# Kernel optimization log

Hardware: AMD Instinct MI355X
Metric: run time of the kernel (lower is better)

Reference implementation:

```python
import jax, jax.numpy as jnp
import numpy as np

TOP_K = 2
ROUTE_SCALE = 1.0
EPS = 1e-20

B, S, D = 2, 512, 1024
E = 8            # num_experts
F = 768          # moe_intermediate_size
FS = 768 * 1     # shared expert intermediate (moe_intermediate_size * num_shared_experts)


def setup_inputs() -> dict:
    key = jax.random.key(0)
    ks = jax.random.split(key, 9)
    s = 0.02
    return {
        "hidden_states": jax.random.normal(ks[0], (B, S, D), dtype=jnp.float32),
        "W_gate_router": jax.random.normal(ks[1], (D, E), dtype=jnp.float32) * s,
        "expert_bias": jnp.zeros((E,), dtype=jnp.float32),
        "Wg": jax.random.normal(ks[2], (E, D, F), dtype=jnp.float32) * s,
        "Wu": jax.random.normal(ks[3], (E, D, F), dtype=jnp.float32) * s,
        "Wd": jax.random.normal(ks[4], (E, F, D), dtype=jnp.float32) * s,
        "Wg_s": jax.random.normal(ks[5], (D, FS), dtype=jnp.float32) * s,
        "Wu_s": jax.random.normal(ks[6], (D, FS), dtype=jnp.float32) * s,
        "Wd_s": jax.random.normal(ks[7], (FS, D), dtype=jnp.float32) * s,
    }


def reference(hidden_states, W_gate_router, expert_bias, Wg, Wu, Wd, Wg_s, Wu_s, Wd_s):
    b, s, d = hidden_states.shape
    x = hidden_states.reshape(-1, d)                      # [T, D]
    T = x.shape[0]

    # ---- token-choice top-k router (sigmoid scoring, route_norm) ----
    logits = x @ W_gate_router                            # [T, E]
    scores = jax.nn.sigmoid(logits.astype(jnp.float32))   # [T, E] fp32
    _, sel = jax.lax.top_k(scores + expert_bias, TOP_K)   # [T, K] (bias only for selection)
    top_scores = jnp.take_along_axis(scores, sel, axis=1)  # [T, K]
    top_scores = top_scores / (top_scores.sum(-1, keepdims=True) + EPS)  # route_norm
    top_scores = top_scores * ROUTE_SCALE

    # ---- shared expert (always active) ----
    shared = (jax.nn.silu(x @ Wg_s) * (x @ Wu_s)) @ Wd_s  # [T, D]

    # ---- dispatch: N = T*K routed slots (scatter-add is order-independent,
    #      so the torch stable-argsort grouping is mathematically a no-op) ----
    tok = jnp.repeat(jnp.arange(T), TOP_K)                # [N] source token per slot
    exp = sel.reshape(-1)                                 # [N] expert per slot
    w = top_scores.reshape(-1)                            # [N]
    xr = x[tok]                                           # [N, D]

    # per-expert SiLU-GLU MLP, vectorized over experts then select own expert's row
    h = jax.nn.silu(jnp.einsum('nd,edf->enf', xr, Wg)) * jnp.einsum('nd,edf->enf', xr, Wu)
    out_all = jnp.einsum('enf,efd->end', h, Wd)           # [E, N, D]
    routed = out_all[exp, jnp.arange(exp.shape[0])]       # [N, D]
    routed = (routed.astype(jnp.float32) * w[:, None]).astype(hidden_states.dtype)

    # ---- combine: scatter-add routed outputs onto shared output ----
    out = shared.at[tok].add(routed)                      # [T, D]
    return out.reshape(b, s, d)
```

## Files before the change

kernel.cpp:

```cpp
#include <hip/hip_runtime.h>
#include <hip/hip_bf16.h>
#include <math.h>

#define T_TOK   1024
#define D_DIM   1024
#define E_NUM   8
#define F_DIM   768
#define N_SLOTS 2048

typedef unsigned short u16;
typedef unsigned int   u32;
typedef __attribute__((ext_vector_type(8))) short bf16x8;
typedef __attribute__((ext_vector_type(4))) float f32x4;

#define WS_SEL    0
#define WS_WTS    8192
#define WS_BUCKET 16384
#define WS_COUNTS 49152
#define WS_OFFS   49216
#define WS_POS    49280
#define WS_XB     65536
#define WS_H      (WS_XB + 2097152)
#define WS_Y      (WS_H + 4718592)

__device__ __forceinline__ u16 f2bf(float x) {
    u32 u = __float_as_uint(x);
    u += 0x7fffu + ((u >> 16) & 1u);
    return (u16)(u >> 16);
}
#define PKBF(hi, lo) __builtin_amdgcn_perm(__float_as_uint(hi), __float_as_uint(lo), 0x07060302u)

__device__ __forceinline__ int physB(int r, int c) {
    return r * 64 + ((c ^ (r & 7)) << 3);
}

__global__ __launch_bounds__(256) void xrouter_kernel(
    const float* __restrict__ X, const float* __restrict__ Wr,
    const float* __restrict__ bias, u16* __restrict__ Xb,
    int* __restrict__ sel, float* __restrict__ wts)
{
    int t = blockIdx.x * 4 + (threadIdx.x >> 6);
    int lane = threadIdx.x & 63;
    const float* xrow = X + (size_t)t * D_DIM;
    u16* brow = Xb + (size_t)t * D_DIM;
    float acc[E_NUM];
#pragma unroll
    for (int e = 0; e < E_NUM; ++e) acc[e] = 0.f;
#pragma unroll
    for (int q = 0; q < 4; ++q) {
        int d = q * 256 + lane * 4;
        float4 v = *(const float4*)(xrow + d);
        ushort4 o;
        o.x = f2bf(v.x); o.y = f2bf(v.y); o.z = f2bf(v.z); o.w = f2bf(v.w);
        *(ushort4*)(brow + d) = o;
        const float xv[4] = {v.x, v.y, v.z, v.w};
#pragma unroll
        for (int jj = 0; jj < 4; ++jj) {
            const float4* wr = (const float4*)(Wr + (size_t)(d + jj) * E_NUM);
            float4 w0 = wr[0], w1 = wr[1];
            acc[0] += xv[jj] * w0.x; acc[1] += xv[jj] * w0.y;
            acc[2] += xv[jj] * w0.z; acc[3] += xv[jj] * w0.w;
            acc[4] += xv[jj] * w1.x; acc[5] += xv[jj] * w1.y;
            acc[6] += xv[jj] * w1.z; acc[7] += xv[jj] * w1.w;
        }
    }
#pragma unroll
    for (int e = 0; e < E_NUM; ++e)
#pragma unroll
        for (int off = 32; off > 0; off >>= 1)
            acc[e] += __shfl_xor(acc[e], off);
    if (lane == 0) {
        float s[E_NUM], b[E_NUM];
#pragma unroll
        for (int e = 0; e < E_NUM; ++e) {
            s[e] = 1.f / (1.f + expf(-acc[e]));
            b[e] = s[e] + bias[e];
        }
        int i1 = 0; float b1 = b[0];
#pragma unroll
        for (int e = 1; e < E_NUM; ++e) if (b[e] > b1) { b1 = b[e]; i1 = e; }
        int i2 = -1; float b2 = -INFINITY;
#pragma unroll
        for (int e = 0; e < E_NUM; ++e) {
            if (e == i1) continue;
            if (b[e] > b2) { b2 = b[e]; i2 = e; }
        }
        float s1 = s[i1], s2 = s[i2];
        float denom = s1 + s2 + 1e-20f;
        sel[2 * t] = i1; sel[2 * t + 1] = i2;
        wts[2 * t] = s1 / denom; wts[2 * t + 1] = s2 / denom;
    }
}

__global__ __launch_bounds__(512) void dispatch_kernel(
    const int* __restrict__ sel, int* __restrict__ bucket,
    int* __restrict__ counts, int* __restrict__ offs, int* __restrict__ pos)
{
    __shared__ int soffs[E_NUM + 1];
    int e = threadIdx.x >> 6;
    int lane = threadIdx.x & 63;
    int running = 0;
    for (int base = 0; base < N_SLOTS; base += 64) {
        int slot = base + lane;
        bool mine = (sel[slot] == e);
        unsigned long long mask = __ballot(mine);
        if (mine) {
            int rank = running + __popcll(mask & ((1ull << lane) - 1ull));
            bucket[e * T_TOK + rank] = slot;
        }
        running += __popcll(mask);
    }
    if (lane == 0) counts[e] = running;
    __syncthreads();
    if (threadIdx.x == 0) {
        int o = 0;
        for (int k = 0; k < E_NUM; ++k) { soffs[k] = o; offs[k] = o; o += counts[k]; }
        soffs[E_NUM] = o; offs[E_NUM] = o;
    }
    __syncthreads();
    int base_off = soffs[e];
    for (int r = lane; r < running; r += 64)
        pos[bucket[e * T_TOK + r]] = base_off + r;
}

__global__ __launch_bounds__(256, 4) void proj1(
    const u16* __restrict__ Xb,
    const float* __restrict__ Wg, const float* __restrict__ Wu,
    const float* __restrict__ Wgs, const float* __restrict__ Wus,
    u16* __restrict__ H,
    const int* __restrict__ bucket, const int* __restrict__ counts, const int* __restrict__ offs)
{
    const int i = blockIdx.x;
    const int cxcd = i & 7, m = i >> 3;
    const int y = m & 31, phi = m >> 5;
    const int panel = phi * 8 + cxcd;
    if (panel >= 108) return;
    const int unit = panel / 12, x = panel - unit * 12;

    int nrows, rbase; const float *Bg, *Bu;
    if (unit < E_NUM) {
        nrows = counts[unit]; rbase = offs[unit];
        Bg = Wg + (size_t)unit * D_DIM * F_DIM;
        Bu = Wu + (size_t)unit * D_DIM * F_DIM;
    } else { nrows = T_TOK; rbase = N_SLOTS; Bg = Wgs; Bu = Wus; }
    const int row0 = y * 32;
    if (row0 >= nrows) return;

    __shared__ u16 smem[2][160 * 64];

    const int t = threadIdx.x;
    const int wv = t >> 6, lane = t & 63, l15 = lane & 15, g = lane >> 4;

    const int ar = t >> 3, ac = t & 7;
    int grow = min(row0 + ar, nrows - 1);
    if (unit < E_NUM) grow = bucket[unit * T_TOK + grow] >> 1;
    const u16* srcA = Xb + (size_t)grow * D_DIM + ac * 8;
    const int wA = physB(ar, ac);

    const int bn = t & 127, bh = t >> 7;
    const float* srcB = ((bn < 64) ? Bg : Bu) + (size_t)(bh * 32) * F_DIM + x * 64 + (bn & 63);
    int wB[4];
#pragma unroll
    for (int q = 0; q < 4; ++q)
        wB[q] = physB(32 + bn, bh * 4 + q);

    f32x4 accg[2], accu[2];
    const f32x4 z4 = {0.f, 0.f, 0.f, 0.f};
#pragma unroll
    for (int ri = 0; ri < 2; ++ri) { accg[ri] = z4; accu[ri] = z4; }

    uint4 pa;
    float pb[32];
#define LOAD1(kt) do { \
    pa = *(const uint4*)(srcA + (kt)); \
    const float* _bp = srcB + (size_t)(kt) * F_DIM; \
    _Pragma("unroll") \
    for (int ii = 0; ii < 32; ++ii) pb[ii] = _bp[(size_t)ii * F_DIM]; \
} while (0)
#define WRITE1(buf) do { \
    *(uint4*)&smem[buf][wA] = pa; \
    _Pragma("unroll") \
    for (int q = 0; q < 4; ++q) { \
        u32 pk[4]; \
        _Pragma("unroll") \
        for (int j = 0; j < 4; ++j) pk[j] = PKBF(pb[8*q + 2*j + 1], pb[8*q + 2*j]); \
        *(uint4*)&smem[buf][wB[q]] = *(const uint4*)pk; \
    } \
} while (0)
#define COMP1(buf) do { \
    const u16* _p = smem[buf]; \
    _Pragma("unroll") \
    for (int kk = 0; kk < 2; ++kk) { \
        bf16x8 _a[2], _bg, _bu; \
        _Pragma("unroll") \
        for (int ri = 0; ri < 2; ++ri) { \
            int rr = ri * 16 + l15; \
            _a[ri] = *(const bf16x8*)&_p[rr * 64 + ((((kk << 2) | g) ^ (rr & 7)) << 3)]; \
        } \
        { \
            int rg = 32 + wv * 16 + l15; \
            _bg = *(const bf16x8*)&_p[rg * 64 + ((((kk << 2) | g) ^ (rg & 7)) << 3)]; \
            int ru = rg + 64; \
            _bu = *(const bf16x8*)&_p[ru * 64 + ((((kk << 2) | g) ^ (ru & 7)) << 3)]; \
        } \
        _Pragma("unroll") \
        for (int ri = 0; ri < 2; ++ri) { \
            accg[ri] = __builtin_amdgcn_mfma_f32_16x16x32_bf16(_a[ri], _bg, accg[ri], 0, 0, 0); \
            accu[ri] = __builtin_amdgcn_mfma_f32_16x16x32_bf16(_a[ri], _bu, accu[ri], 0, 0, 0); \
        } \
    } \
} while (0)

    LOAD1(0);
    for (int tt = 0; tt < 16; ++tt) {
        WRITE1(tt & 1);
        if (tt + 1 < 16) LOAD1((tt + 1) * 64);
        __syncthreads();
        COMP1(tt & 1);
    }
#undef LOAD1
#undef WRITE1
#undef COMP1

#pragma unroll
    for (int ri = 0; ri < 2; ++ri) {
        int n = x * 64 + wv * 16 + l15;
#pragma unroll
        for (int r = 0; r < 4; ++r) {
            int row = row0 + ri * 16 + g * 4 + r;
            if (row >= nrows) continue;
            float gv = accg[ri][r];
            float uv = accu[ri][r];
            H[(size_t)(rbase + row) * F_DIM + n] =
                f2bf(gv / (1.f + __expf(-gv)) * uv);
        }
    }
}

__global__ __launch_bounds__(256, 3) void proj2(
    const u16* __restrict__ H,
    const float* __restrict__ Wd, const float* __restrict__ Wds,
    float* __restrict__ Y,
    const int* __restrict__ counts, const int* __restrict__ offs)
{
    const int i = blockIdx.x;
    const int cxcd = i & 7, m = i >> 3;
    const int y = m & 31, phi = m >> 5;
    const int panel = phi * 8 + cxcd;
    const int unit = panel >> 4, x = panel & 15;

    int nrows, rbase; const float* Bm;
    if (unit < E_NUM) {
        nrows = counts[unit]; rbase = offs[unit];
        Bm = Wd + (size_t)unit * F_DIM * D_DIM;
    } else { nrows = T_TOK; rbase = N_SLOTS; Bm = Wds; }
    const int row0 = y * 64;
    if (row0 >= nrows) return;

    __shared__ u16 smem[2][128 * 64];

    const int t = threadIdx.x;
    const int wv = t >> 6, lane = t & 63, l15 = lane & 15, g = lane >> 4;
    const int wm = wv >> 1, wn = wv & 1;

    const int ar = t >> 2, ac = t & 3;
    const int grow = rbase + min(row0 + ar, nrows - 1);
    const u16* srcA = H + (size_t)grow * F_DIM + ac * 8;
    const int wA0 = ar * 64 + ((ac     ^ (ar & 7)) * 8);
    const int wA1 = ar * 64 + (((ac+4) ^ (ar & 7)) * 8);

    const int bn = t & 63;
    const int bq = t >> 6;
    const float* srcB = Bm + (size_t)(bq * 16) * D_DIM + x * 64 + bn;
    int wB[2];
#pragma unroll
    for (int q = 0; q < 2; ++q)
        wB[q] = (64 + bn) * 64 + (((bq * 2 + q) ^ (bn & 7)) * 8);

    f32x4 acc[2][2];
    const f32x4 z4 = {0.f, 0.f, 0.f, 0.f};
#pragma unroll
    for (int ri = 0; ri < 2; ++ri)
#pragma unroll
        for (int ci = 0; ci < 2; ++ci) acc[ri][ci] = z4;

    uint4 pa0, pa1;
    float pb[16];
#define LOAD2(kt) do { \
    pa0 = *(const uint4*)(srcA + (kt)); \
    pa1 = *(const uint4*)(srcA + (kt) + 32); \
    const float* _bp = srcB + (size_t)(kt) * D_DIM; \
    _Pragma("unroll") \
    for (int ii = 0; ii < 16; ++ii) pb[ii] = _bp[(size_t)ii * D_DIM]; \
} while (0)
#define WRITE2(buf) do { \
    *(uint4*)&smem[buf][wA0] = pa0; \
    *(uint4*)&smem[buf][wA1] = pa1; \
    _Pragma("unroll") \
    for (int q = 0; q < 2; ++q) { \
        u32 pk[4]; \
        _Pragma("unroll") \
        for (int j = 0; j < 4; ++j) pk[j] = PKBF(pb[8*q + 2*j + 1], pb[8*q + 2*j]); \
        *(uint4*)&smem[buf][wB[q]] = *(const uint4*)pk; \
    } \
} while (0)
#define COMP2(buf) do { \
    const u16* _p = smem[buf]; \
    _Pragma("unroll") \
    for (int kk = 0; kk < 2; ++kk) { \
        const int ch = (((kk << 2) | g) ^ (l15 & 7)) * 8; \
        bf16x8 _a[2], _b[2]; \
        _Pragma("unroll") \
        for (int ri = 0; ri < 2; ++ri) \
            _a[ri] = *(const bf16x8*)&_p[(wm * 32 + ri * 16 + l15) * 64 + ch]; \
        _Pragma("unroll") \
        for (int ci = 0; ci < 2; ++ci) \
            _b[ci] = *(const bf16x8*)&_p[(64 + wn * 32 + ci * 16 + l15) * 64 + ch]; \
        _Pragma("unroll") \
        for (int ri = 0; ri < 2; ++ri) \
            _Pragma("unroll") \
            for (int ci = 0; ci < 2; ++ci) \
                acc[ri][ci] = __builtin_amdgcn_mfma_f32_16x16x32_bf16(_a[ri], _b[ci], acc[ri][ci], 0, 0, 0); \
    } \
} while (0)

    LOAD2(0);
    for (int tt = 0; tt < 12; ++tt) {
        WRITE2(tt & 1);
        if (tt + 1 < 12) LOAD2((tt + 1) * 64);
        __syncthreads();
        COMP2(tt & 1);
    }
#undef LOAD2
#undef WRITE2
#undef COMP2

#pragma unroll
    for (int ri = 0; ri < 2; ++ri)
#pragma unroll
        for (int ci = 0; ci < 2; ++ci) {
            int n = x * 64 + wn * 32 + ci * 16 + l15;
#pragma unroll
            for (int r = 0; r < 4; ++r) {
                int row = row0 + wm * 32 + ri * 16 + g * 4 + r;
                if (row >= nrows) continue;
                Y[(size_t)(rbase + row) * D_DIM + n] = acc[ri][ci][r];
            }
        }
}

__global__ __launch_bounds__(256) void combine_kernel(
    const float* __restrict__ Y, const int* __restrict__ pos,
    const float* __restrict__ wts, float* __restrict__ out)
{
    int t = blockIdx.x;
    int d = threadIdx.x * 4;
    int p0 = pos[2 * t], p1 = pos[2 * t + 1];
    float w0 = wts[2 * t], w1 = wts[2 * t + 1];
    float4 a = *(const float4*)(Y + (size_t)(N_SLOTS + t) * D_DIM + d);
    float4 b = *(const float4*)(Y + (size_t)p0 * D_DIM + d);
    float4 cc = *(const float4*)(Y + (size_t)p1 * D_DIM + d);
    float4 o;
    o.x = a.x + w0 * b.x + w1 * cc.x;
    o.y = a.y + w0 * b.y + w1 * cc.y;
    o.z = a.z + w0 * b.z + w1 * cc.z;
    o.w = a.w + w0 * b.w + w1 * cc.w;
    *(float4*)(out + (size_t)t * D_DIM + d) = o;
}

extern "C" void kernel_launch(void* const* d_in, const int* in_sizes, int n_in,
                              void* d_out, int out_size, void* d_ws, size_t ws_size,
                              hipStream_t stream) {
    const float* X    = (const float*)d_in[0];
    const float* Wr   = (const float*)d_in[1];
    const float* bias = (const float*)d_in[2];
    const float* Wg   = (const float*)d_in[3];
    const float* Wu   = (const float*)d_in[4];
    const float* Wd   = (const float*)d_in[5];
    const float* Wgs  = (const float*)d_in[6];
    const float* Wus  = (const float*)d_in[7];
    const float* Wds  = (const float*)d_in[8];
    float* out = (float*)d_out;

    char* ws = (char*)d_ws;
    int*   sel    = (int*)(ws + WS_SEL);
    float* wtsv   = (float*)(ws + WS_WTS);
    int*   bucket = (int*)(ws + WS_BUCKET);
    int*   counts = (int*)(ws + WS_COUNTS);
    int*   offs   = (int*)(ws + WS_OFFS);
    int*   pos    = (int*)(ws + WS_POS);
    u16*   Xb     = (u16*)(ws + WS_XB);
    u16*   H      = (u16*)(ws + WS_H);
    float* Y      = (float*)(ws + WS_Y);

    xrouter_kernel<<<256, 256, 0, stream>>>(X, Wr, bias, Xb, sel, wtsv);
    dispatch_kernel<<<1, 512, 0, stream>>>(sel, bucket, counts, offs, pos);

    proj1<<<3584, 256, 0, stream>>>(Xb, Wg, Wu, Wgs, Wus, H, bucket, counts, offs);
    proj2<<<4608, 256, 0, stream>>>(H, Wd, Wds, Y, counts, offs);
    combine_kernel<<<T_TOK, 256, 0, stream>>>(Y, pos, wtsv, out);
}
```

Baseline: 92.25 us.

## Swap GEMM operand roles with weight-stationary tiles and async LDS token loads

Both expert GEMMs are restructured so each block owns a weight column slice and a 256-token tile, with the weights as the small M operand and tokens as N. Token activations are copied straight into LDS with global_load_lds, and the fp32 weight loads overlap compute in a reordered double-buffer loop. Per-block tiles grow a lot (fewer blocks, more accumulators, vectorized stores), cutting how often the fp32 weights are re-read across token tiles. The cost is lower occupancy, larger LDS use, and idle waves in partially filled expert tiles.

```diff
diff --git a/kernel.cpp b/kernel.cpp
--- a/kernel.cpp
+++ b/kernel.cpp
@@ -32,6 +32,12 @@
 
 __device__ __forceinline__ int physB(int r, int c) {
     return r * 64 + ((c ^ (r & 7)) << 3);
+}
+
+__device__ __forceinline__ void async16(const void* gp, void* sp) {
+    __builtin_amdgcn_global_load_lds(
+        (const __attribute__((address_space(1))) unsigned int*)gp,
+        (__attribute__((address_space(3))) unsigned int*)sp, 16, 0, 0);
 }
 
 __global__ __launch_bounds__(256) void xrouter_kernel(
@@ -123,19 +129,19 @@
         pos[bucket[e * T_TOK + r]] = base_off + r;
 }
 
-__global__ __launch_bounds__(256, 4) void proj1(
+__global__ __launch_bounds__(256, 2) void proj1(
     const u16* __restrict__ Xb,
     const float* __restrict__ Wg, const float* __restrict__ Wu,
     const float* __restrict__ Wgs, const float* __restrict__ Wus,
     u16* __restrict__ H,
-    const int* __restrict__ bucket, const int* __restrict__ counts, const int* __restrict__ offs)
+    const int* __restrict__ bucket, const int* __restrict__ counts,
+    const int* __restrict__ offs)
 {
     const int i = blockIdx.x;
-    const int cxcd = i & 7, m = i >> 3;
-    const int y = m & 31, phi = m >> 5;
-    const int panel = phi * 8 + cxcd;
-    if (panel >= 108) return;
-    const int unit = panel / 12, x = panel - unit * 12;
+    const int unit = i / 96;
+    const int rem = i - unit * 96;
+    const int x = rem >> 2;
+    const int nt = rem & 3;
 
     int nrows, rbase; const float *Bg, *Bu;
     if (unit < E_NUM) {
@@ -143,209 +149,217 @@
         Bg = Wg + (size_t)unit * D_DIM * F_DIM;
         Bu = Wu + (size_t)unit * D_DIM * F_DIM;
     } else { nrows = T_TOK; rbase = N_SLOTS; Bg = Wgs; Bu = Wus; }
-    const int row0 = y * 32;
-    if (row0 >= nrows) return;
-
-    __shared__ u16 smem[2][160 * 64];
-
-    const int t = threadIdx.x;
-    const int wv = t >> 6, lane = t & 63, l15 = lane & 15, g = lane >> 4;
-
-    const int ar = t >> 3, ac = t & 7;
-    int grow = min(row0 + ar, nrows - 1);
-    if (unit < E_NUM) grow = bucket[unit * T_TOK + grow] >> 1;
-    const u16* srcA = Xb + (size_t)grow * D_DIM + ac * 8;
-    const int wA = physB(ar, ac);
-
-    const int bn = t & 127, bh = t >> 7;
-    const float* srcB = ((bn < 64) ? Bg : Bu) + (size_t)(bh * 32) * F_DIM + x * 64 + (bn & 63);
-    int wB[4];
-#pragma unroll
-    for (int q = 0; q < 4; ++q)
-        wB[q] = physB(32 + bn, bh * 4 + q);
-
-    f32x4 accg[2], accu[2];
+    const int tbase = nt * 256;
+    if (tbase >= nrows) return;
+
+    __shared__ u16 smem[2][320 * 64];
+
+    const int t = threadIdx.x, wv = t >> 6, lane = t & 63, l15 = lane & 15, g = lane >> 4;
+
+    const float* srcA = ((lane < 32) ? Bg : Bu) + (size_t)(wv * 16) * F_DIM + x * 32 + (lane & 31);
+    const int wA0 = physB(lane, 2 * wv);
+    const int wA1 = physB(lane, 2 * wv + 1);
+
+    const u16* srcB[8];
+#pragma unroll
+    for (int j = 0; j < 8; ++j) {
+        int tl = wv * 64 + j * 8 + (lane >> 3);
+        int tok = min(tbase + tl, nrows - 1);
+        int grow = (unit < E_NUM) ? (bucket[unit * T_TOK + tok] >> 1) : tok;
+        srcB[j] = Xb + (size_t)grow * D_DIM + (((lane & 7) ^ (lane >> 3)) << 3);
+    }
+
+    f32x4 accg[2][4], accu[2][4];
     const f32x4 z4 = {0.f, 0.f, 0.f, 0.f};
 #pragma unroll
-    for (int ri = 0; ri < 2; ++ri) { accg[ri] = z4; accu[ri] = z4; }
-
-    uint4 pa;
-    float pb[32];
-#define LOAD1(kt) do { \
-    pa = *(const uint4*)(srcA + (kt)); \
-    const float* _bp = srcB + (size_t)(kt) * F_DIM; \
-    _Pragma("unroll") \
-    for (int ii = 0; ii < 32; ++ii) pb[ii] = _bp[(size_t)ii * F_DIM]; \
-} while (0)
-#define WRITE1(buf) do { \
-    *(uint4*)&smem[buf][wA] = pa; \
-    _Pragma("unroll") \
-    for (int q = 0; q < 4; ++q) { \
-        u32 pk[4]; \
-        _Pragma("unroll") \
-        for (int j = 0; j < 4; ++j) pk[j] = PKBF(pb[8*q + 2*j + 1], pb[8*q + 2*j]); \
-        *(uint4*)&smem[buf][wB[q]] = *(const uint4*)pk; \
-    } \
+    for (int mi = 0; mi < 2; ++mi)
+#pragma unroll
+        for (int ni = 0; ni < 4; ++ni) { accg[mi][ni] = z4; accu[mi][ni] = z4; }
+
+    float pa[16];
+#define ASYNCB1(kt, buf) do { \
+    _Pragma("unroll") \
+    for (int j = 0; j < 8; ++j) \
+        async16(srcB[j] + (kt), &smem[buf][(64 + wv * 64 + j * 8) * 64]); \
+} while (0)
+#define LOADA1(kt) do { \
+    const float* _s = srcA + (size_t)(kt) * F_DIM; \
+    _Pragma("unroll") \
+    for (int j = 0; j < 16; ++j) pa[j] = _s[(size_t)j * F_DIM]; \
+} while (0)
+#define WRITEA1(buf) do { \
+    u32 pk[8]; \
+    _Pragma("unroll") \
+    for (int j = 0; j < 8; ++j) pk[j] = PKBF(pa[2*j + 1], pa[2*j]); \
+    *(uint4*)&smem[buf][wA0] = *(const uint4*)&pk[0]; \
+    *(uint4*)&smem[buf][wA1] = *(const uint4*)&pk[4]; \
 } while (0)
 #define COMP1(buf) do { \
     const u16* _p = smem[buf]; \
     _Pragma("unroll") \
     for (int kk = 0; kk < 2; ++kk) { \
-        bf16x8 _a[2], _bg, _bu; \
-        _Pragma("unroll") \
-        for (int ri = 0; ri < 2; ++ri) { \
-            int rr = ri * 16 + l15; \
-            _a[ri] = *(const bf16x8*)&_p[rr * 64 + ((((kk << 2) | g) ^ (rr & 7)) << 3)]; \
+        const int ch = (((kk << 2) | g) ^ (l15 & 7)) << 3; \
+        bf16x8 _ag[2], _au[2], _b[4]; \
+        _Pragma("unroll") \
+        for (int mi = 0; mi < 2; ++mi) { \
+            _ag[mi] = *(const bf16x8*)&_p[(mi * 16 + l15) * 64 + ch]; \
+            _au[mi] = *(const bf16x8*)&_p[(32 + mi * 16 + l15) * 64 + ch]; \
         } \
-        { \
-            int rg = 32 + wv * 16 + l15; \
-            _bg = *(const bf16x8*)&_p[rg * 64 + ((((kk << 2) | g) ^ (rg & 7)) << 3)]; \
-            int ru = rg + 64; \
-            _bu = *(const bf16x8*)&_p[ru * 64 + ((((kk << 2) | g) ^ (ru & 7)) << 3)]; \
-        } \
-        _Pragma("unroll") \
-        for (int ri = 0; ri < 2; ++ri) { \
-            accg[ri] = __builtin_amdgcn_mfma_f32_16x16x32_bf16(_a[ri], _bg, accg[ri], 0, 0, 0); \
-            accu[ri] = __builtin_amdgcn_mfma_f32_16x16x32_bf16(_a[ri], _bu, accu[ri], 0, 0, 0); \
-        } \
+        _Pragma("unroll") \
+        for (int ni = 0; ni < 4; ++ni) \
+            _b[ni] = *(const bf16x8*)&_p[(64 + wv * 64 + ni * 16 + l15) * 64 + ch]; \
+        _Pragma("unroll") \
+        for (int mi = 0; mi < 2; ++mi) \
+            _Pragma("unroll") \
+            for (int ni = 0; ni < 4; ++ni) { \
+                accg[mi][ni] = __builtin_amdgcn_mfma_f32_16x16x32_bf16(_ag[mi], _b[ni], accg[mi][ni], 0, 0, 0); \
+                accu[mi][ni] = __builtin_amdgcn_mfma_f32_16x16x32_bf16(_au[mi], _b[ni], accu[mi][ni], 0, 0, 0); \
+            } \
     } \
 } while (0)
 
-    LOAD1(0);
+    ASYNCB1(0, 0);
+    LOADA1(0);
+    WRITEA1(0);
+    __syncthreads();
     for (int tt = 0; tt < 16; ++tt) {
-        WRITE1(tt & 1);
-        if (tt + 1 < 16) LOAD1((tt + 1) * 64);
+        const int cb = tt & 1, nb = cb ^ 1;
+        if (tt + 1 < 16) { ASYNCB1((tt + 1) * 64, nb); LOADA1((tt + 1) * 64); }
+        COMP1(cb);
+        if (tt + 1 < 16) WRITEA1(nb);
         __syncthreads();
-        COMP1(tt & 1);
-    }
-#undef LOAD1
-#undef WRITE1
+    }
+#undef ASYNCB1
+#undef LOADA1
+#undef WRITEA1
 #undef COMP1
 
 #pragma unroll
-    for (int ri = 0; ri < 2; ++ri) {
-        int n = x * 64 + wv * 16 + l15;
-#pragma unroll
-        for (int r = 0; r < 4; ++r) {
-            int row = row0 + ri * 16 + g * 4 + r;
-            if (row >= nrows) continue;
-            float gv = accg[ri][r];
-            float uv = accu[ri][r];
-            H[(size_t)(rbase + row) * F_DIM + n] =
-                f2bf(gv / (1.f + __expf(-gv)) * uv);
-        }
-    }
-}
-
-__global__ __launch_bounds__(256, 3) void proj2(
+    for (int mi = 0; mi < 2; ++mi)
+#pragma unroll
+        for (int ni = 0; ni < 4; ++ni) {
+            int token = tbase + wv * 64 + ni * 16 + l15;
+            if (token >= nrows) continue;
+            int f0 = x * 32 + mi * 16 + g * 4;
+            ushort4 hv;
+            float gv, uv;
+            gv = accg[mi][ni][0]; uv = accu[mi][ni][0];
+            hv.x = f2bf(gv / (1.f + __expf(-gv)) * uv);
+            gv = accg[mi][ni][1]; uv = accu[mi][ni][1];
+            hv.y = f2bf(gv / (1.f + __expf(-gv)) * uv);
+            gv = accg[mi][ni][2]; uv = accu[mi][ni][2];
+            hv.z = f2bf(gv / (1.f + __expf(-gv)) * uv);
+            gv = accg[mi][ni][3]; uv = accu[mi][ni][3];
+            hv.w = f2bf(gv / (1.f + __expf(-gv)) * uv);
+            *(ushort4*)(H + (size_t)(rbase + token) * F_DIM + f0) = hv;
+        }
+}
+
+__global__ __launch_bounds__(256, 2) void proj2(
     const u16* __restrict__ H,
     const float* __restrict__ Wd, const float* __restrict__ Wds,
     float* __restrict__ Y,
     const int* __restrict__ counts, const int* __restrict__ offs)
 {
     const int i = blockIdx.x;
-    const int cxcd = i & 7, m = i >> 3;
-    const int y = m & 31, phi = m >> 5;
-    const int panel = phi * 8 + cxcd;
-    const int unit = panel >> 4, x = panel & 15;
+    const int unit = i / 64;
+    const int rem = i - unit * 64;
+    const int x = rem >> 2;
+    const int nt = rem & 3;
 
     int nrows, rbase; const float* Bm;
     if (unit < E_NUM) {
         nrows = counts[unit]; rbase = offs[unit];
         Bm = Wd + (size_t)unit * F_DIM * D_DIM;
     } else { nrows = T_TOK; rbase = N_SLOTS; Bm = Wds; }
-    const int row0 = y * 64;
-    if (row0 >= nrows) return;
-
-    __shared__ u16 smem[2][128 * 64];
-
-    const int t = threadIdx.x;
-    const int wv = t >> 6, lane = t & 63, l15 = lane & 15, g = lane >> 4;
-    const int wm = wv >> 1, wn = wv & 1;
-
-    const int ar = t >> 2, ac = t & 3;
-    const int grow = rbase + min(row0 + ar, nrows - 1);
-    const u16* srcA = H + (size_t)grow * F_DIM + ac * 8;
-    const int wA0 = ar * 64 + ((ac     ^ (ar & 7)) * 8);
-    const int wA1 = ar * 64 + (((ac+4) ^ (ar & 7)) * 8);
-
-    const int bn = t & 63;
-    const int bq = t >> 6;
-    const float* srcB = Bm + (size_t)(bq * 16) * D_DIM + x * 64 + bn;
-    int wB[2];
-#pragma unroll
-    for (int q = 0; q < 2; ++q)
-        wB[q] = (64 + bn) * 64 + (((bq * 2 + q) ^ (bn & 7)) * 8);
-
-    f32x4 acc[2][2];
+    const int tbase = nt * 256;
+    if (tbase >= nrows) return;
+
+    __shared__ u16 smem[2][320 * 64];
+
+    const int t = threadIdx.x, wv = t >> 6, lane = t & 63, l15 = lane & 15, g = lane >> 4;
+
+    const float* srcA = Bm + (size_t)(wv * 16) * D_DIM + x * 64 + lane;
+    const int wA0 = physB(lane, 2 * wv);
+    const int wA1 = physB(lane, 2 * wv + 1);
+
+    const u16* srcB[8];
+#pragma unroll
+    for (int j = 0; j < 8; ++j) {
+        int tl = wv * 64 + j * 8 + (lane >> 3);
+        int tok = min(tbase + tl, nrows - 1);
+        srcB[j] = H + (size_t)(rbase + tok) * F_DIM + (((lane & 7) ^ (lane >> 3)) << 3);
+    }
+
+    f32x4 acc[4][4];
     const f32x4 z4 = {0.f, 0.f, 0.f, 0.f};
 #pragma unroll
-    for (int ri = 0; ri < 2; ++ri)
-#pragma unroll
-        for (int ci = 0; ci < 2; ++ci) acc[ri][ci] = z4;
-
-    uint4 pa0, pa1;
-    float pb[16];
-#define LOAD2(kt) do { \
-    pa0 = *(const uint4*)(srcA + (kt)); \
-    pa1 = *(const uint4*)(srcA + (kt) + 32); \
-    const float* _bp = srcB + (size_t)(kt) * D_DIM; \
-    _Pragma("unroll") \
-    for (int ii = 0; ii < 16; ++ii) pb[ii] = _bp[(size_t)ii * D_DIM]; \
-} while (0)
-#define WRITE2(buf) do { \
-    *(uint4*)&smem[buf][wA0] = pa0; \
-    *(uint4*)&smem[buf][wA1] = pa1; \
-    _Pragma("unroll") \
-    for (int q = 0; q < 2; ++q) { \
-        u32 pk[4]; \
-        _Pragma("unroll") \
-        for (int j = 0; j < 4; ++j) pk[j] = PKBF(pb[8*q + 2*j + 1], pb[8*q + 2*j]); \
-        *(uint4*)&smem[buf][wB[q]] = *(const uint4*)pk; \
-    } \
+    for (int mi = 0; mi < 4; ++mi)
+#pragma unroll
+        for (int ni = 0; ni < 4; ++ni) acc[mi][ni] = z4;
+
+    float pa[16];
+#define ASYNCB2(kt, buf) do { \
+    _Pragma("unroll") \
+    for (int j = 0; j < 8; ++j) \
+        async16(srcB[j] + (kt), &smem[buf][(64 + wv * 64 + j * 8) * 64]); \
+} while (0)
+#define LOADA2(kt) do { \
+    const float* _s = srcA + (size_t)(kt) * D_DIM; \
+    _Pragma("unroll") \
+    for (int j = 0; j < 16; ++j) pa[j] = _s[(size_t)j * D_DIM]; \
+} while (0)
+#define WRITEA2(buf) do { \
+    u32 pk[8]; \
+    _Pragma("unroll") \
+    for (int j = 0; j < 8; ++j) pk[j] = PKBF(pa[2*j + 1], pa[2*j]); \
+    *(uint4*)&smem[buf][wA0] = *(const uint4*)&pk[0]; \
+    *(uint4*)&smem[buf][wA1] = *(const uint4*)&pk[4]; \
 } while (0)
 #define COMP2(buf) do { \
     const u16* _p = smem[buf]; \
     _Pragma("unroll") \
     for (int kk = 0; kk < 2; ++kk) { \
-        const int ch = (((kk << 2) | g) ^ (l15 & 7)) * 8; \
-        bf16x8 _a[2], _b[2]; \
-        _Pragma("unroll") \
-        for (int ri = 0; ri < 2; ++ri) \
-            _a[ri] = *(const bf16x8*)&_p[(wm * 32 + ri * 16 + l15) * 64 + ch]; \
-        _Pragma("unroll") \
-        for (int ci = 0; ci < 2; ++ci) \
-            _b[ci] = *(const bf16x8*)&_p[(64 + wn * 32 + ci * 16 + l15) * 64 + ch]; \
-        _Pragma("unroll") \
-        for (int ri = 0; ri < 2; ++ri) \
+        const int ch = (((kk << 2) | g) ^ (l15 & 7)) << 3; \
+        bf16x8 _a[4], _b[4]; \
+        _Pragma("unroll") \
+        for (int mi = 0; mi < 4; ++mi) \
+            _a[mi] = *(const bf16x8*)&_p[(mi * 16 + l15) * 64 + ch]; \
+        _Pragma("unroll") \
+        for (int ni = 0; ni < 4; ++ni) \
+            _b[ni] = *(const bf16x8*)&_p[(64 + wv * 64 + ni * 16 + l15) * 64 + ch]; \
+        _Pragma("unroll") \
+        for (int mi = 0; mi < 4; ++mi) \
             _Pragma("unroll") \
-            for (int ci = 0; ci < 2; ++ci) \
-                acc[ri][ci] = __builtin_amdgcn_mfma_f32_16x16x32_bf16(_a[ri], _b[ci], acc[ri][ci], 0, 0, 0); \
+            for (int ni = 0; ni < 4; ++ni) \
+                acc[mi][ni] = __builtin_amdgcn_mfma_f32_16x16x32_bf16(_a[mi], _b[ni], acc[mi][ni], 0, 0, 0); \
     } \
 } while (0)
 
-    LOAD2(0);
+    ASYNCB2(0, 0);
+    LOADA2(0);
+    WRITEA2(0);
+    __syncthreads();
     for (int tt = 0; tt < 12; ++tt) {
-        WRITE2(tt & 1);
-        if (tt + 1 < 12) LOAD2((tt + 1) * 64);
+        const int cb = tt & 1, nb = cb ^ 1;
+        if (tt + 1 < 12) { ASYNCB2((tt + 1) * 64, nb); LOADA2((tt + 1) * 64); }
+        COMP2(cb);
+        if (tt + 1 < 12) WRITEA2(nb);
         __syncthreads();
-        COMP2(tt & 1);
-    }
-#undef LOAD2
-#undef WRITE2
+    }
+#undef ASYNCB2
+#undef LOADA2
+#undef WRITEA2
 #undef COMP2
 
 #pragma unroll
-    for (int ri = 0; ri < 2; ++ri)
-#pragma unroll
-        for (int ci = 0; ci < 2; ++ci) {
-            int n = x * 64 + wn * 32 + ci * 16 + l15;
-#pragma unroll
-            for (int r = 0; r < 4; ++r) {
-                int row = row0 + wm * 32 + ri * 16 + g * 4 + r;
-                if (row >= nrows) continue;
-                Y[(size_t)(rbase + row) * D_DIM + n] = acc[ri][ci][r];
-            }
+    for (int mi = 0; mi < 4; ++mi)
+#pragma unroll
+        for (int ni = 0; ni < 4; ++ni) {
+            int token = tbase + wv * 64 + ni * 16 + l15;
+            if (token >= nrows) continue;
+            int d0 = x * 64 + mi * 16 + g * 4;
+            *(f32x4*)(Y + (size_t)(rbase + token) * D_DIM + d0) = acc[mi][ni];
         }
 }
 
@@ -396,7 +410,7 @@
     xrouter_kernel<<<256, 256, 0, stream>>>(X, Wr, bias, Xb, sel, wtsv);
     dispatch_kernel<<<1, 512, 0, stream>>>(sel, bucket, counts, offs, pos);
 
-    proj1<<<3584, 256, 0, stream>>>(Xb, Wg, Wu, Wgs, Wus, H, bucket, counts, offs);
-    proj2<<<4608, 256, 0, stream>>>(H, Wd, Wds, Y, counts, offs);
+    proj1<<<864, 256, 0, stream>>>(Xb, Wg, Wu, Wgs, Wus, H, bucket, counts, offs);
+    proj2<<<576, 256, 0, stream>>>(H, Wd, Wds, Y, counts, offs);
     combine_kernel<<<T_TOK, 256, 0, stream>>>(Y, pos, wtsv, out);
 }
```

Result: slower. 131.7 us (+42.7%).
